# Kernel tuning notes

Measured on AMD Instinct MI355X. Metric: run time of the kernel, lower is better.

The kernel has to match this reference:

```python
import jax, jax.numpy as jnp
import numpy as np

N, K, F, NRBF = 10000, 32, 128, 300
GAMMA = 10.0


def ssp(x):
    # shifted softplus: softplus(x) - log(2)
    return jax.nn.softplus(x) - jnp.log(2.0).astype(x.dtype)


def setup_inputs() -> dict:
    key = jax.random.key(0)
    ks = jax.random.split(key, 12)
    s = lambda fan_in: 1.0 / np.sqrt(fan_in)
    inp = {
        "xyz": jax.random.normal(ks[0], (N, 3), jnp.float32) * 5.0,
        "atomic": jax.random.normal(ks[1], (N, F), jnp.float32),
        "edge_mask": (jax.random.uniform(ks[2], (N, K)) < 0.9).astype(jnp.float32),
        "src": jax.random.randint(ks[3], (N, K), 0, N),
        # pre_conv Linear(F, F) with bias
        "W_pre": jax.random.uniform(ks[4], (F, F), jnp.float32, -s(F), s(F)),
        "b_pre": jax.random.uniform(ks[5], (F,), jnp.float32, -s(F), s(F)),
        # cfconv: Linear(300, F, bias=False), SSP, Linear(F, F, bias=False), SSP
        "W_cf1": jax.random.uniform(ks[6], (NRBF, F), jnp.float32, -s(NRBF), s(NRBF)),
        "W_cf2": jax.random.uniform(ks[7], (F, F), jnp.float32, -s(F), s(F)),
        # post_conv: Linear(F,F), SSP, Linear(F,F)
        "W_post1": jax.random.uniform(ks[8], (F, F), jnp.float32, -s(F), s(F)),
        "b_post1": jax.random.uniform(ks[9], (F,), jnp.float32, -s(F), s(F)),
        "W_post2": jax.random.uniform(ks[10], (F, F), jnp.float32, -s(F), s(F)),
        "b_post2": jax.random.uniform(ks[11], (F,), jnp.float32, -s(F), s(F)),
        "rbf_centers": jnp.linspace(0.1, 30.1, NRBF, dtype=jnp.float32),
    }
    return inp


def reference(xyz, atomic, edge_mask, src, W_pre, b_pre, W_cf1, W_cf2,
              W_post1, b_post1, W_post2, b_post2, rbf_centers):
    pre = atomic @ W_pre + b_pre                       # [N, F]
    nbr_xyz = xyz[src]                                 # gather: [N, K, 3]
    d_ij = jnp.linalg.norm(nbr_xyz - xyz[:, None, :], axis=2, keepdims=True)  # [N, K, 1]
    rbf = jnp.exp(-GAMMA * (d_ij - rbf_centers[None, None, :]) ** 2)          # [N, K, 300]
    filters = ssp(ssp(rbf @ W_cf1) @ W_cf2)            # [N, K, F]
    conv_out = jnp.sum(filters * pre[src] * edge_mask[:, :, None], axis=1)    # [N, F]
    post = ssp(conv_out @ W_post1 + b_post1) @ W_post2 + b_post2
    return atomic + post
```

## Files before the change

### kernel.cpp

```cpp
#include <hip/hip_runtime.h>

#define NATOMS 10000
#define KNB 32
#define FD 128
#define NRBF 300
#define STEPC (30.0f / 299.0f)
#define INVSTEP (299.0f / 30.0f)
#define TROWS 256

typedef short short8 __attribute__((ext_vector_type(8)));
typedef float f32x4 __attribute__((ext_vector_type(4)));
typedef unsigned int u32x4 __attribute__((ext_vector_type(4)));

__device__ __forceinline__ unsigned short f2bf_rne(float f) {
    unsigned int u = __float_as_uint(f);
    u = (u + 0x7fffu + ((u >> 16) & 1u)) >> 16;
    return (unsigned short)u;
}

__device__ __forceinline__ unsigned int pack_bf2(float hi, float lo) {
    return __builtin_amdgcn_perm(__float_as_uint(hi) + 0x8000u,
                                 __float_as_uint(lo) + 0x8000u, 0x07060302u);
}

__device__ __forceinline__ unsigned short f2bf_rhu(float f) {
    return (unsigned short)((__float_as_uint(f) + 0x8000u) >> 16);
}

__device__ __forceinline__ float ssp_fast(float x) {
    float t = __builtin_amdgcn_exp2f(x * 1.44269504f);
    float l = __builtin_amdgcn_logf(1.0f + t);
    return 0.69314718056f * (l - 1.0f);
}

__device__ __forceinline__ float ssp_poly(float x) {
    float u = x * x;
    float p = fmaf(u, 2.1356923e-6f, -2.6351976e-5f);
    p = fmaf(u, p, 3.2552083e-4f);
    p = fmaf(u, p, -5.2083333e-3f);
    p = fmaf(u, p, 0.125f);
    return fmaf(0.5f, x, u * p);
}

__device__ __forceinline__ void gload_lds16(const void* g, void* l) {
    __builtin_amdgcn_global_load_lds(
        (const __attribute__((address_space(1))) unsigned int*)g,
        (__attribute__((address_space(3))) unsigned int*)l, 16, 0, 0);
}

__device__ __forceinline__ short8 rbf_row8(float d, float cg) {
    float t = d - cg;
    t = fminf(3.5f, fmaxf(-3.5f, t));
    float r = __builtin_amdgcn_exp2f(-14.4269504f * t * t);
    float q = __builtin_amdgcn_exp2f((28.8539008f * STEPC) * t
                                     - (14.4269504f * STEPC * STEPC));
    const float QRATIO = 0.81763172f;
    u32x4 p;
#pragma unroll
    for (int jj = 0; jj < 4; ++jj) {
        float v0 = r; r *= q; q *= QRATIO;
        float v1 = r; r *= q; q *= QRATIO;
        p[jj] = pack_bf2(v1, v0);
    }
    return __builtin_bit_cast(short8, p);
}

__global__ __launch_bounds__(256) void prep_pack(
    const float* __restrict__ Wcf1, const float* __restrict__ Wpre,
    const float* __restrict__ Wcf2, const float* __restrict__ Wpost1,
    const float* __restrict__ Wpost2, unsigned short* __restrict__ w1p,
    unsigned short* __restrict__ w4p) {
    int idx = blockIdx.x * 256 + threadIdx.x;
    if (idx < 40960) {
        int j = idx & 7, c = (idx >> 3) & 127, g = (idx >> 10) & 3, kc = idx >> 12;
        int k = kc * 32 + g * 8 + j;
        float v = (k < NRBF) ? Wcf1[k * FD + c] : 0.f;
        w1p[idx] = f2bf_rne(v);
    } else if (idx < 40960 + 65536) {
        int t = idx - 40960;
        int sel = t >> 14;
        int t2 = t & 16383;
        int j = t2 & 7, c = (t2 >> 3) & 127, g = (t2 >> 10) & 3, kc = t2 >> 12;
        int k = kc * 32 + g * 8 + j;
        const float* W = (sel == 0) ? Wpre : (sel == 1) ? Wcf2 : (sel == 2) ? Wpost1 : Wpost2;
        w4p[t] = f2bf_rne(W[k * FD + c]);
    }
}

__global__ __launch_bounds__(256) void pre_and_table(
    const float* __restrict__ X, const unsigned short* __restrict__ Wp,
    const float* __restrict__ bias, unsigned int* __restrict__ preP,
    const unsigned short* __restrict__ w1p, const unsigned short* __restrict__ w2p,
    unsigned int* __restrict__ T) {
    __shared__ unsigned short A2[128][132];
    const int tid = threadIdx.x;
    const int w = tid >> 6, lane = tid & 63, g = lane >> 4, c16 = lane & 15;

    if (blockIdx.x < 157) {
        const int r0 = blockIdx.x * 64 + w * 16;
        f32x4 acc[8];
#pragma unroll
        for (int b = 0; b < 8; ++b) acc[b] = (f32x4){0.f, 0.f, 0.f, 0.f};
        int row = r0 + c16;
        if (row >= NATOMS) row = 0;
#pragma unroll
        for (int kc = 0; kc < 4; ++kc) {
            const float* p0 = X + (size_t)row * FD + kc * 32 + g * 8;
            float4 xa = *(const float4*)p0, xb = *(const float4*)(p0 + 4);
            u32x4 pa;
            pa[0] = pack_bf2(xa.y, xa.x); pa[1] = pack_bf2(xa.w, xa.z);
            pa[2] = pack_bf2(xb.y, xb.x); pa[3] = pack_bf2(xb.w, xb.z);
            short8 a0 = __builtin_bit_cast(short8, pa);
            const unsigned short* wb = Wp + (kc * 4 + g) * 1024 + c16 * 8;
#pragma unroll
            for (int nb = 0; nb < 8; ++nb) {
                short8 b = *(const short8*)(wb + nb * 128);
                acc[nb] = __builtin_amdgcn_mfma_f32_16x16x32_bf16(a0, b, acc[nb], 0, 0, 0);
            }
        }
        float bv[8];
#pragma unroll
        for (int nb = 0; nb < 8; ++nb) bv[nb] = bias[nb * 16 + c16];
#pragma unroll
        for (int q = 0; q < 4; ++q) {
            int orow = r0 + 4 * g + q;
            if (orow < NATOMS) {
#pragma unroll
                for (int p2 = 0; p2 < 4; ++p2) {
                    float v0 = acc[2 * p2][q] + bv[2 * p2];
                    float v1 = acc[2 * p2 + 1][q] + bv[2 * p2 + 1];
                    preP[orow * 64 + c16 * 4 + p2] = pack_bf2(v1, v0);
                }
            }
        }
        return;
    }

    const int rbase = (int)(blockIdx.x - 157) * 128 + w * 32;
    const float hstep = 0.125f;
    const float d0 = (float)(rbase + c16) * hstep;
    const float d1 = (float)(rbase + 16 + c16) * hstep;

    const float BAND = 1.05f;
    float lo = (float)rbase * hstep, hi = (float)(rbase + 31) * hstep;
    int L = max(0, (int)floorf(((lo - BAND - 0.1f) * INVSTEP - 31.f) * 0.03125f));
    int H = min(9, (int)floorf(((hi + BAND - 0.1f) * INVSTEP) * 0.03125f));

    f32x4 acc[2][8];
#pragma unroll
    for (int a = 0; a < 2; ++a)
#pragma unroll
        for (int b = 0; b < 8; ++b) acc[a][b] = (f32x4){0.f, 0.f, 0.f, 0.f};

    for (int kc = L; kc <= H; ++kc) {
        const unsigned short* wb = w1p + kc * 4096 + g * 1024 + c16 * 8;
        short8 bfr[8];
#pragma unroll
        for (int nb = 0; nb < 8; ++nb) bfr[nb] = *(const short8*)(wb + nb * 128);
        const float cg = 0.1f + (float)(kc * 32 + g * 8) * STEPC;
        short8 a0 = rbf_row8(d0, cg);
        short8 a1 = rbf_row8(d1, cg);
#pragma unroll
        for (int nb = 0; nb < 8; ++nb) {
            acc[0][nb] = __builtin_amdgcn_mfma_f32_16x16x32_bf16(a0, bfr[nb], acc[0][nb], 0, 0, 0);
            acc[1][nb] = __builtin_amdgcn_mfma_f32_16x16x32_bf16(a1, bfr[nb], acc[1][nb], 0, 0, 0);
        }
    }

#pragma unroll
    for (int mr = 0; mr < 2; ++mr)
#pragma unroll
        for (int nb = 0; nb < 8; ++nb)
#pragma unroll
            for (int q = 0; q < 4; ++q) {
                int row = w * 32 + mr * 16 + 4 * g + q;
                A2[row][nb * 16 + c16] = f2bf_rhu(ssp_poly(acc[mr][nb][q]));
            }

    f32x4 acc2[2][8];
#pragma unroll
    for (int a = 0; a < 2; ++a)
#pragma unroll
        for (int b = 0; b < 8; ++b) acc2[a][b] = (f32x4){0.f, 0.f, 0.f, 0.f};

#pragma unroll
    for (int kc = 0; kc < 4; ++kc) {
        short8 a0 = *(const short8*)&A2[w * 32 + c16][kc * 32 + g * 8];
        short8 a1 = *(const short8*)&A2[w * 32 + 16 + c16][kc * 32 + g * 8];
        const unsigned short* wb = w2p + (kc * 4 + g) * 1024 + c16 * 8;
#pragma unroll
        for (int nb = 0; nb < 8; ++nb) {
            short8 b = *(const short8*)(wb + nb * 128);
            acc2[0][nb] = __builtin_amdgcn_mfma_f32_16x16x32_bf16(a0, b, acc2[0][nb], 0, 0, 0);
            acc2[1][nb] = __builtin_amdgcn_mfma_f32_16x16x32_bf16(a1, b, acc2[1][nb], 0, 0, 0);
        }
    }

#pragma unroll
    for (int mr = 0; mr < 2; ++mr)
#pragma unroll
        for (int q = 0; q < 4; ++q) {
            int r = rbase + mr * 16 + 4 * g + q;
#pragma unroll
            for (int p2 = 0; p2 < 4; ++p2) {
                float F0 = ssp_poly(acc2[mr][2 * p2][q]);
                float F1 = ssp_poly(acc2[mr][2 * p2 + 1][q]);
                T[r * 64 + c16 * 4 + p2] =
                    ((unsigned int)f2bf_rne(F1) << 16) | f2bf_rne(F0);
            }
        }
}

__global__ __launch_bounds__(512, 2) void conv_post(
    const float* __restrict__ xyz, const int* __restrict__ src,
    const float* __restrict__ mask, const unsigned int* __restrict__ preP,
    const unsigned int* __restrict__ T, const unsigned short* __restrict__ w1,
    const float* __restrict__ b1, const unsigned short* __restrict__ w2,
    const float* __restrict__ b2, const float* __restrict__ resid,
    float* __restrict__ Y) {
    __shared__ unsigned int Tl[TROWS * 64];
    __shared__ unsigned short Aconv[16][132];

    const int tid = threadIdx.x;
    const int w = tid >> 6;
    const int lane = tid & 63;
    const int l5 = lane & 31;
    const int c16 = lane & 15;
    const int g = lane >> 4;

#pragma unroll
    for (int it = 0; it < 8; ++it) {
        const unsigned int* gp = T + w * 2048 + it * 256 + lane * 4;
        gload_lds16(gp, &Tl[w * 2048 + it * 256]);
    }

    const int iA = blockIdx.x * 16 + w;
    const int iB = iA + 8;

    int svA = src[iA * KNB + l5];
    int svB = src[iB * KNB + l5];
    float mvA = mask[iA * KNB + l5];
    float mvB = mask[iB * KNB + l5];
    float dxA = xyz[3 * svA]     - xyz[3 * iA];
    float dyA = xyz[3 * svA + 1] - xyz[3 * iA + 1];
    float dzA = xyz[3 * svA + 2] - xyz[3 * iA + 2];
    float dxB = xyz[3 * svB]     - xyz[3 * iB];
    float dyB = xyz[3 * svB + 1] - xyz[3 * iB + 1];
    float dzB = xyz[3 * svB + 2] - xyz[3 * iB + 2];
    float dA = sqrtf(dxA * dxA + dyA * dyA + dzA * dzA);
    float dB = sqrtf(dxB * dxB + dyB * dyB + dzB * dzB);
    dA = (mvA > 0.f) ? dA : 1e9f;
    dB = (mvB > 0.f) ? dB : 1e9f;
    float tA = fminf(dA * 8.0f, (float)(TROWS - 2) + 0.999f);
    float tB = fminf(dB * 8.0f, (float)(TROWS - 2) + 0.999f);
    float fiA = floorf(tA), fiB = floorf(tB);
    float frA = tA - fiA,  frB = tB - fiB;
    int iiA = (int)fiA, iiB = (int)fiB;

    __syncthreads();

    float a00 = 0.f, a01 = 0.f, a10 = 0.f, a11 = 0.f;
#pragma unroll
    for (int e = 0; e < KNB; ++e) {
        int   ie0 = __builtin_amdgcn_readlane(iiA, e);
        int   se0 = __builtin_amdgcn_readlane(svA, e);
        float fe0 = __uint_as_float((unsigned int)__builtin_amdgcn_readlane(
                        (int)__float_as_uint(frA), e));
        int   ie1 = __builtin_amdgcn_readlane(iiB, e);
        int   se1 = __builtin_amdgcn_readlane(svB, e);
        float fe1 = __uint_as_float((unsigned int)__builtin_amdgcn_readlane(
                        (int)__float_as_uint(frB), e));
        unsigned int tvA0 = Tl[ie0 * 64 + lane];
        unsigned int tvB0 = Tl[ie0 * 64 + 64 + lane];
        unsigned int tvA1 = Tl[ie1 * 64 + lane];
        unsigned int tvB1 = Tl[ie1 * 64 + 64 + lane];
        unsigned int pw0 = preP[se0 * 64 + lane];
        unsigned int pw1 = preP[se1 * 64 + lane];
        float A00 = __uint_as_float(tvA0 << 16);
        float A01 = __uint_as_float(tvA0 & 0xffff0000u);
        float B00 = __uint_as_float(tvB0 << 16);
        float B01 = __uint_as_float(tvB0 & 0xffff0000u);
        float f00 = fmaf(fe0, B00 - A00, A00);
        float f01 = fmaf(fe0, B01 - A01, A01);
        a00 = fmaf(f00, __uint_as_float(pw0 << 16), a00);
        a01 = fmaf(f01, __uint_as_float(pw0 & 0xffff0000u), a01);
        float A10 = __uint_as_float(tvA1 << 16);
        float A11 = __uint_as_float(tvA1 & 0xffff0000u);
        float B10 = __uint_as_float(tvB1 << 16);
        float B11 = __uint_as_float(tvB1 & 0xffff0000u);
        float f10 = fmaf(fe1, B10 - A10, A10);
        float f11 = fmaf(fe1, B11 - A11, A11);
        a10 = fmaf(f10, __uint_as_float(pw1 << 16), a10);
        a11 = fmaf(f11, __uint_as_float(pw1 & 0xffff0000u), a11);
    }
    {
        int c0 = 32 * (lane & 3) + (lane >> 2);
        Aconv[w][c0]          = f2bf_rhu(a00);
        Aconv[w][c0 + 16]     = f2bf_rhu(a01);
        Aconv[w + 8][c0]      = f2bf_rhu(a10);
        Aconv[w + 8][c0 + 16] = f2bf_rhu(a11);
    }
    __syncthreads();

    unsigned short* Amid = (unsigned short*)Tl;
    const int r0 = blockIdx.x * 16;

    f32x4 acc = (f32x4){0.f, 0.f, 0.f, 0.f};
#pragma unroll
    for (int kc = 0; kc < 4; ++kc) {
        short8 a0 = *(const short8*)&Aconv[c16][kc * 32 + g * 8];
        const unsigned short* wb = w1 + (kc * 4 + g) * 1024;
        short8 b = *(const short8*)(wb + (w * 16 + c16) * 8);
        acc = __builtin_amdgcn_mfma_f32_16x16x32_bf16(a0, b, acc, 0, 0, 0);
    }
    {
        float bv = b1[w * 16 + c16];
#pragma unroll
        for (int q = 0; q < 4; ++q)
            Amid[(4 * g + q) * 132 + w * 16 + c16] =
                f2bf_rhu(ssp_fast(acc[q] + bv));
    }
    __syncthreads();

    f32x4 acc2 = (f32x4){0.f, 0.f, 0.f, 0.f};
#pragma unroll
    for (int kc = 0; kc < 4; ++kc) {
        short8 a0 = *(const short8*)&Amid[c16 * 132 + kc * 32 + g * 8];
        const unsigned short* wb = w2 + (kc * 4 + g) * 1024;
        short8 b = *(const short8*)(wb + (w * 16 + c16) * 8);
        acc2 = __builtin_amdgcn_mfma_f32_16x16x32_bf16(a0, b, acc2, 0, 0, 0);
    }
    {
        float bv2 = b2[w * 16 + c16];
#pragma unroll
        for (int q = 0; q < 4; ++q) {
            int o = (r0 + 4 * g + q) * FD + w * 16 + c16;
            Y[o] = acc2[q] + bv2 + resid[o];
        }
    }
}

extern "C" void kernel_launch(void* const* d_in, const int* in_sizes, int n_in,
                              void* d_out, int out_size, void* d_ws, size_t ws_size,
                              hipStream_t stream) {
    const float* xyz     = (const float*)d_in[0];
    const float* atomic  = (const float*)d_in[1];
    const float* mask    = (const float*)d_in[2];
    const int*   src     = (const int*)d_in[3];
    const float* W_pre   = (const float*)d_in[4];
    const float* b_pre   = (const float*)d_in[5];
    const float* W_cf1   = (const float*)d_in[6];
    const float* W_cf2   = (const float*)d_in[7];
    const float* W_post1 = (const float*)d_in[8];
    const float* b_post1 = (const float*)d_in[9];
    const float* W_post2 = (const float*)d_in[10];
    const float* b_post2 = (const float*)d_in[11];
    float* out = (float*)d_out;

    unsigned int*   preP = (unsigned int*)d_ws;
    unsigned short* w1p  = (unsigned short*)((char*)d_ws + 7680000);
    unsigned short* w4p  = w1p + 40960;
    unsigned int*   T    = (unsigned int*)((char*)d_ws + 7892992);
    unsigned short* wpre   = w4p;
    unsigned short* wcf2   = w4p + 16384;
    unsigned short* wpost1 = w4p + 32768;
    unsigned short* wpost2 = w4p + 49152;

    prep_pack<<<416, 256, 0, stream>>>(W_cf1, W_pre, W_cf2, W_post1, W_post2, w1p, w4p);
    pre_and_table<<<159, 256, 0, stream>>>(atomic, wpre, b_pre, preP, w1p, wcf2, T);
    conv_post<<<625, 512, 0, stream>>>(xyz, src, mask, preP, T,
                                       wpost1, b_post1, wpost2, b_post2, atomic, out);
}
```

Before: 40.27 us.

## Fold weight packing into pre/table kernel and batch neighbor gathers

Removes the separate weight-packing kernel. The pre-linear and RBF-table blocks now read fp32 weights directly and convert them to bf16 fragments on the fly. Dedicated extra blocks pack the post weights, and the pre GEMM is split across twice as many blocks with half the output columns per wave. The conv loop is restructured to issue eight neighbors' table and preP loads before consuming them, which raises memory-level parallelism at the cost of more registers. The changes cut one kernel launch but add strided, uncoalesced fp32 weight reads inside the compute kernels.

```diff
diff --git a/kernel.cpp b/kernel.cpp
--- a/kernel.cpp
+++ b/kernel.cpp
@@ -65,44 +65,50 @@
     return __builtin_bit_cast(short8, p);
 }
 
-__global__ __launch_bounds__(256) void prep_pack(
-    const float* __restrict__ Wcf1, const float* __restrict__ Wpre,
-    const float* __restrict__ Wcf2, const float* __restrict__ Wpost1,
-    const float* __restrict__ Wpost2, unsigned short* __restrict__ w1p,
-    unsigned short* __restrict__ w4p) {
-    int idx = blockIdx.x * 256 + threadIdx.x;
-    if (idx < 40960) {
-        int j = idx & 7, c = (idx >> 3) & 127, g = (idx >> 10) & 3, kc = idx >> 12;
-        int k = kc * 32 + g * 8 + j;
-        float v = (k < NRBF) ? Wcf1[k * FD + c] : 0.f;
-        w1p[idx] = f2bf_rne(v);
-    } else if (idx < 40960 + 65536) {
-        int t = idx - 40960;
-        int sel = t >> 14;
-        int t2 = t & 16383;
-        int j = t2 & 7, c = (t2 >> 3) & 127, g = (t2 >> 10) & 3, kc = t2 >> 12;
-        int k = kc * 32 + g * 8 + j;
-        const float* W = (sel == 0) ? Wpre : (sel == 1) ? Wcf2 : (sel == 2) ? Wpost1 : Wpost2;
-        w4p[t] = f2bf_rne(W[k * FD + c]);
-    }
-}
-
-__global__ __launch_bounds__(256) void pre_and_table(
-    const float* __restrict__ X, const unsigned short* __restrict__ Wp,
+__device__ __forceinline__ short8 load_bfrag_f32(const float* __restrict__ W,
+                                                 int k0, int c) {
+    u32x4 p;
+#pragma unroll
+    for (int jj = 0; jj < 4; ++jj) {
+        int ka = k0 + 2 * jj;
+        p[jj] = pack_bf2(W[(ka + 1) * FD + c], W[ka * FD + c]);
+    }
+    return __builtin_bit_cast(short8, p);
+}
+
+__device__ __forceinline__ short8 load_bfrag_f32_g(const float* __restrict__ W,
+                                                   int k0, int c, int kmax) {
+    u32x4 p;
+#pragma unroll
+    for (int jj = 0; jj < 4; ++jj) {
+        int ka = k0 + 2 * jj;
+        float va = (ka < kmax) ? W[ka * FD + c] : 0.f;
+        float vb = (ka + 1 < kmax) ? W[(ka + 1) * FD + c] : 0.f;
+        p[jj] = pack_bf2(vb, va);
+    }
+    return __builtin_bit_cast(short8, p);
+}
+
+__global__ __launch_bounds__(256) void pre_table_pack(
+    const float* __restrict__ X, const float* __restrict__ Wpre,
     const float* __restrict__ bias, unsigned int* __restrict__ preP,
-    const unsigned short* __restrict__ w1p, const unsigned short* __restrict__ w2p,
-    unsigned int* __restrict__ T) {
+    const float* __restrict__ Wcf1, const float* __restrict__ Wcf2,
+    unsigned int* __restrict__ T, const float* __restrict__ Wpost1,
+    const float* __restrict__ Wpost2, unsigned short* __restrict__ wp) {
     __shared__ unsigned short A2[128][132];
     const int tid = threadIdx.x;
     const int w = tid >> 6, lane = tid & 63, g = lane >> 4, c16 = lane & 15;
 
-    if (blockIdx.x < 157) {
-        const int r0 = blockIdx.x * 64 + w * 16;
-        f32x4 acc[8];
-#pragma unroll
-        for (int b = 0; b < 8; ++b) acc[b] = (f32x4){0.f, 0.f, 0.f, 0.f};
-        int row = r0 + c16;
+    if (blockIdx.x < 313) {
+        const int r0b = blockIdx.x * 32;
+        const int r = w >> 1, c = w & 1;
+        int row = r0b + r * 16 + c16;
         if (row >= NATOMS) row = 0;
+
+        f32x4 acc[4];
+#pragma unroll
+        for (int b = 0; b < 4; ++b) acc[b] = (f32x4){0.f, 0.f, 0.f, 0.f};
+
 #pragma unroll
         for (int kc = 0; kc < 4; ++kc) {
             const float* p0 = X + (size_t)row * FD + kc * 32 + g * 8;
@@ -111,32 +117,45 @@
             pa[0] = pack_bf2(xa.y, xa.x); pa[1] = pack_bf2(xa.w, xa.z);
             pa[2] = pack_bf2(xb.y, xb.x); pa[3] = pack_bf2(xb.w, xb.z);
             short8 a0 = __builtin_bit_cast(short8, pa);
-            const unsigned short* wb = Wp + (kc * 4 + g) * 1024 + c16 * 8;
-#pragma unroll
-            for (int nb = 0; nb < 8; ++nb) {
-                short8 b = *(const short8*)(wb + nb * 128);
+            int k0 = kc * 32 + g * 8;
+#pragma unroll
+            for (int nb = 0; nb < 4; ++nb) {
+                short8 b = load_bfrag_f32(Wpre, k0, (c * 4 + nb) * 16 + c16);
                 acc[nb] = __builtin_amdgcn_mfma_f32_16x16x32_bf16(a0, b, acc[nb], 0, 0, 0);
             }
         }
-        float bv[8];
-#pragma unroll
-        for (int nb = 0; nb < 8; ++nb) bv[nb] = bias[nb * 16 + c16];
+
+        float bv[4];
+#pragma unroll
+        for (int nb = 0; nb < 4; ++nb) bv[nb] = bias[(c * 4 + nb) * 16 + c16];
 #pragma unroll
         for (int q = 0; q < 4; ++q) {
-            int orow = r0 + 4 * g + q;
+            int orow = r0b + r * 16 + 4 * g + q;
             if (orow < NATOMS) {
 #pragma unroll
-                for (int p2 = 0; p2 < 4; ++p2) {
-                    float v0 = acc[2 * p2][q] + bv[2 * p2];
-                    float v1 = acc[2 * p2 + 1][q] + bv[2 * p2 + 1];
-                    preP[orow * 64 + c16 * 4 + p2] = pack_bf2(v1, v0);
+                for (int pp = 0; pp < 2; ++pp) {
+                    float v0 = acc[2 * pp][q] + bv[2 * pp];
+                    float v1 = acc[2 * pp + 1][q] + bv[2 * pp + 1];
+                    preP[orow * 64 + c16 * 4 + c * 2 + pp] = pack_bf2(v1, v0);
                 }
             }
         }
         return;
     }
 
-    const int rbase = (int)(blockIdx.x - 157) * 128 + w * 32;
+    if (blockIdx.x >= 315) {
+        const int sel = blockIdx.x - 315;
+        const float* W = sel ? Wpost2 : Wpost1;
+        unsigned short* o = wp + sel * 16384;
+        for (int t2 = tid; t2 < 16384; t2 += 256) {
+            int j = t2 & 7, cc = (t2 >> 3) & 127, gg = (t2 >> 10) & 3, kc = t2 >> 12;
+            int k = kc * 32 + gg * 8 + j;
+            o[t2] = f2bf_rne(W[k * FD + cc]);
+        }
+        return;
+    }
+
+    const int rbase = (int)(blockIdx.x - 313) * 128 + w * 32;
     const float hstep = 0.125f;
     const float d0 = (float)(rbase + c16) * hstep;
     const float d1 = (float)(rbase + 16 + c16) * hstep;
@@ -153,11 +172,12 @@
         for (int b = 0; b < 8; ++b) acc[a][b] = (f32x4){0.f, 0.f, 0.f, 0.f};
 
     for (int kc = L; kc <= H; ++kc) {
-        const unsigned short* wb = w1p + kc * 4096 + g * 1024 + c16 * 8;
+        int k0 = kc * 32 + g * 8;
         short8 bfr[8];
 #pragma unroll
-        for (int nb = 0; nb < 8; ++nb) bfr[nb] = *(const short8*)(wb + nb * 128);
-        const float cg = 0.1f + (float)(kc * 32 + g * 8) * STEPC;
+        for (int nb = 0; nb < 8; ++nb)
+            bfr[nb] = load_bfrag_f32_g(Wcf1, k0, nb * 16 + c16, NRBF);
+        const float cg = 0.1f + (float)k0 * STEPC;
         short8 a0 = rbf_row8(d0, cg);
         short8 a1 = rbf_row8(d1, cg);
 #pragma unroll
@@ -187,10 +207,9 @@
     for (int kc = 0; kc < 4; ++kc) {
         short8 a0 = *(const short8*)&A2[w * 32 + c16][kc * 32 + g * 8];
         short8 a1 = *(const short8*)&A2[w * 32 + 16 + c16][kc * 32 + g * 8];
-        const unsigned short* wb = w2p + (kc * 4 + g) * 1024 + c16 * 8;
 #pragma unroll
         for (int nb = 0; nb < 8; ++nb) {
-            short8 b = *(const short8*)(wb + nb * 128);
+            short8 b = load_bfrag_f32(Wcf2, kc * 32 + g * 8, nb * 16 + c16);
             acc2[0][nb] = __builtin_amdgcn_mfma_f32_16x16x32_bf16(a0, b, acc2[0][nb], 0, 0, 0);
             acc2[1][nb] = __builtin_amdgcn_mfma_f32_16x16x32_bf16(a1, b, acc2[1][nb], 0, 0, 0);
         }
@@ -200,12 +219,12 @@
     for (int mr = 0; mr < 2; ++mr)
 #pragma unroll
         for (int q = 0; q < 4; ++q) {
-            int r = rbase + mr * 16 + 4 * g + q;
+            int rr = rbase + mr * 16 + 4 * g + q;
 #pragma unroll
             for (int p2 = 0; p2 < 4; ++p2) {
                 float F0 = ssp_poly(acc2[mr][2 * p2][q]);
                 float F1 = ssp_poly(acc2[mr][2 * p2 + 1][q]);
-                T[r * 64 + c16 * 4 + p2] =
+                T[rr * 64 + c16 * 4 + p2] =
                     ((unsigned int)f2bf_rne(F1) << 16) | f2bf_rne(F0);
             }
         }
@@ -261,37 +280,46 @@
 
     float a00 = 0.f, a01 = 0.f, a10 = 0.f, a11 = 0.f;
 #pragma unroll
-    for (int e = 0; e < KNB; ++e) {
-        int   ie0 = __builtin_amdgcn_readlane(iiA, e);
-        int   se0 = __builtin_amdgcn_readlane(svA, e);
-        float fe0 = __uint_as_float((unsigned int)__builtin_amdgcn_readlane(
-                        (int)__float_as_uint(frA), e));
-        int   ie1 = __builtin_amdgcn_readlane(iiB, e);
-        int   se1 = __builtin_amdgcn_readlane(svB, e);
-        float fe1 = __uint_as_float((unsigned int)__builtin_amdgcn_readlane(
-                        (int)__float_as_uint(frB), e));
-        unsigned int tvA0 = Tl[ie0 * 64 + lane];
-        unsigned int tvB0 = Tl[ie0 * 64 + 64 + lane];
-        unsigned int tvA1 = Tl[ie1 * 64 + lane];
-        unsigned int tvB1 = Tl[ie1 * 64 + 64 + lane];
-        unsigned int pw0 = preP[se0 * 64 + lane];
-        unsigned int pw1 = preP[se1 * 64 + lane];
-        float A00 = __uint_as_float(tvA0 << 16);
-        float A01 = __uint_as_float(tvA0 & 0xffff0000u);
-        float B00 = __uint_as_float(tvB0 << 16);
-        float B01 = __uint_as_float(tvB0 & 0xffff0000u);
-        float f00 = fmaf(fe0, B00 - A00, A00);
-        float f01 = fmaf(fe0, B01 - A01, A01);
-        a00 = fmaf(f00, __uint_as_float(pw0 << 16), a00);
-        a01 = fmaf(f01, __uint_as_float(pw0 & 0xffff0000u), a01);
-        float A10 = __uint_as_float(tvA1 << 16);
-        float A11 = __uint_as_float(tvA1 & 0xffff0000u);
-        float B10 = __uint_as_float(tvB1 << 16);
-        float B11 = __uint_as_float(tvB1 & 0xffff0000u);
-        float f10 = fmaf(fe1, B10 - A10, A10);
-        float f11 = fmaf(fe1, B11 - A11, A11);
-        a10 = fmaf(f10, __uint_as_float(pw1 << 16), a10);
-        a11 = fmaf(f11, __uint_as_float(pw1 & 0xffff0000u), a11);
+    for (int eb = 0; eb < KNB; eb += 8) {
+        unsigned int tA0[8], tB0[8], tA1[8], tB1[8], q0[8], q1[8];
+        float fr0[8], fr1[8];
+#pragma unroll
+        for (int j = 0; j < 8; ++j) {
+            const int e = eb + j;
+            int ie0 = __builtin_amdgcn_readlane(iiA, e);
+            int se0 = __builtin_amdgcn_readlane(svA, e);
+            fr0[j] = __uint_as_float((unsigned int)__builtin_amdgcn_readlane(
+                         (int)__float_as_uint(frA), e));
+            int ie1 = __builtin_amdgcn_readlane(iiB, e);
+            int se1 = __builtin_amdgcn_readlane(svB, e);
+            fr1[j] = __uint_as_float((unsigned int)__builtin_amdgcn_readlane(
+                         (int)__float_as_uint(frB), e));
+            q0[j] = preP[se0 * 64 + lane];
+            q1[j] = preP[se1 * 64 + lane];
+            tA0[j] = Tl[ie0 * 64 + lane];
+            tB0[j] = Tl[ie0 * 64 + 64 + lane];
+            tA1[j] = Tl[ie1 * 64 + lane];
+            tB1[j] = Tl[ie1 * 64 + 64 + lane];
+        }
+#pragma unroll
+        for (int j = 0; j < 8; ++j) {
+            float A00 = __uint_as_float(tA0[j] << 16);
+            float A01 = __uint_as_float(tA0[j] & 0xffff0000u);
+            float B00 = __uint_as_float(tB0[j] << 16);
+            float B01 = __uint_as_float(tB0[j] & 0xffff0000u);
+            float f00 = fmaf(fr0[j], B00 - A00, A00);
+            float f01 = fmaf(fr0[j], B01 - A01, A01);
+            a00 = fmaf(f00, __uint_as_float(q0[j] << 16), a00);
+            a01 = fmaf(f01, __uint_as_float(q0[j] & 0xffff0000u), a01);
+            float A10 = __uint_as_float(tA1[j] << 16);
+            float A11 = __uint_as_float(tA1[j] & 0xffff0000u);
+            float B10 = __uint_as_float(tB1[j] << 16);
+            float B11 = __uint_as_float(tB1[j] & 0xffff0000u);
+            float f10 = fmaf(fr1[j], B10 - A10, A10);
+            float f11 = fmaf(fr1[j], B11 - A11, A11);
+            a10 = fmaf(f10, __uint_as_float(q1[j] << 16), a10);
+            a11 = fmaf(f11, __uint_as_float(q1[j] & 0xffff0000u), a11);
+        }
     }
     {
         int c0 = 32 * (lane & 3) + (lane >> 2);
@@ -358,16 +386,11 @@
     float* out = (float*)d_out;
 
     unsigned int*   preP = (unsigned int*)d_ws;
-    unsigned short* w1p  = (unsigned short*)((char*)d_ws + 7680000);
-    unsigned short* w4p  = w1p + 40960;
-    unsigned int*   T    = (unsigned int*)((char*)d_ws + 7892992);
-    unsigned short* wpre   = w4p;
-    unsigned short* wcf2   = w4p + 16384;
-    unsigned short* wpost1 = w4p + 32768;
-    unsigned short* wpost2 = w4p + 49152;
-
-    prep_pack<<<416, 256, 0, stream>>>(W_cf1, W_pre, W_cf2, W_post1, W_post2, w1p, w4p);
-    pre_and_table<<<159, 256, 0, stream>>>(atomic, wpre, b_pre, preP, w1p, wcf2, T);
+    unsigned int*   T    = (unsigned int*)((char*)d_ws + 2560000);
+    unsigned short* wp   = (unsigned short*)((char*)d_ws + 2625536);
+
+    pre_table_pack<<<317, 256, 0, stream>>>(atomic, W_pre, b_pre, preP,
+                                            W_cf1, W_cf2, T, W_post1, W_post2, wp);
     conv_post<<<625, 512, 0, stream>>>(xyz, src, mask, preP, T,
-                                       wpost1, b_post1, wpost2, b_post2, atomic, out);
-}
+                                       wp, b_post1, wp + 16384, b_post2, atomic, out);
+}
```

Measured after the change: 80.94 us. +101.0%, slower.

## Process 20 atoms per conv_post block with 10 waves and a smaller table

Applied to the files above, without the earlier changes.

Shrinks the distance lookup table to 252 rows and changes conv_post to 640-thread blocks that each handle 20 atoms, giving 500 blocks instead of 625. The per-block table load into LDS is spread across 10 waves. The post MLP now runs on 8 waves using two 16-row MFMA tiles over zero-padded rows. This amortises the LDS table fill over more atoms per block and changes occupancy, at the cost of wasted MFMA work on padding rows and two idle waves during the MLP. The workspace layout is also moved.

```diff
diff --git a/kernel.cpp b/kernel.cpp
--- a/kernel.cpp
+++ b/kernel.cpp
@@ -6,7 +6,7 @@
 #define NRBF 300
 #define STEPC (30.0f / 299.0f)
 #define INVSTEP (299.0f / 30.0f)
-#define TROWS 256
+#define TROWS 252
 
 typedef short short8 __attribute__((ext_vector_type(8)));
 typedef float f32x4 __attribute__((ext_vector_type(4)));
@@ -201,17 +201,19 @@
 #pragma unroll
         for (int q = 0; q < 4; ++q) {
             int r = rbase + mr * 16 + 4 * g + q;
-#pragma unroll
-            for (int p2 = 0; p2 < 4; ++p2) {
-                float F0 = ssp_poly(acc2[mr][2 * p2][q]);
-                float F1 = ssp_poly(acc2[mr][2 * p2 + 1][q]);
-                T[r * 64 + c16 * 4 + p2] =
-                    ((unsigned int)f2bf_rne(F1) << 16) | f2bf_rne(F0);
-            }
-        }
-}
-
-__global__ __launch_bounds__(512, 2) void conv_post(
+            if (r < TROWS) {
+#pragma unroll
+                for (int p2 = 0; p2 < 4; ++p2) {
+                    float F0 = ssp_poly(acc2[mr][2 * p2][q]);
+                    float F1 = ssp_poly(acc2[mr][2 * p2 + 1][q]);
+                    T[r * 64 + c16 * 4 + p2] =
+                        ((unsigned int)f2bf_rne(F1) << 16) | f2bf_rne(F0);
+                }
+            }
+        }
+}
+
+__global__ __launch_bounds__(640, 5) void conv_post(
     const float* __restrict__ xyz, const int* __restrict__ src,
     const float* __restrict__ mask, const unsigned int* __restrict__ preP,
     const unsigned int* __restrict__ T, const unsigned short* __restrict__ w1,
@@ -219,7 +221,7 @@
     const float* __restrict__ b2, const float* __restrict__ resid,
     float* __restrict__ Y) {
     __shared__ unsigned int Tl[TROWS * 64];
-    __shared__ unsigned short Aconv[16][132];
+    __shared__ unsigned short Aconv[32][132];
 
     const int tid = threadIdx.x;
     const int w = tid >> 6;
@@ -229,13 +231,17 @@
     const int g = lane >> 4;
 
 #pragma unroll
-    for (int it = 0; it < 8; ++it) {
-        const unsigned int* gp = T + w * 2048 + it * 256 + lane * 4;
-        gload_lds16(gp, &Tl[w * 2048 + it * 256]);
-    }
-
-    const int iA = blockIdx.x * 16 + w;
-    const int iB = iA + 8;
+    for (int it = 0; it < 7; ++it) {
+        int chunk = w * 7 + it;
+        if (chunk < 63) {
+            const unsigned int* gp = T + chunk * 256 + lane * 4;
+            gload_lds16(gp, &Tl[chunk * 256]);
+        }
+    }
+
+    const int base = blockIdx.x * 20;
+    const int iA = base + w;
+    const int iB = iA + 10;
 
     int svA = src[iA * KNB + l5];
     int svB = src[iB * KNB + l5];
@@ -295,48 +301,65 @@
     }
     {
         int c0 = 32 * (lane & 3) + (lane >> 2);
-        Aconv[w][c0]          = f2bf_rhu(a00);
-        Aconv[w][c0 + 16]     = f2bf_rhu(a01);
-        Aconv[w + 8][c0]      = f2bf_rhu(a10);
-        Aconv[w + 8][c0 + 16] = f2bf_rhu(a11);
-    }
+        Aconv[w][c0]           = f2bf_rhu(a00);
+        Aconv[w][c0 + 16]      = f2bf_rhu(a01);
+        Aconv[w + 10][c0]      = f2bf_rhu(a10);
+        Aconv[w + 10][c0 + 16] = f2bf_rhu(a11);
+    }
+
+    for (int idx = tid; idx < 12 * 132; idx += 640)
+        (&Aconv[20][0])[idx] = 0;
+
     __syncthreads();
 
     unsigned short* Amid = (unsigned short*)Tl;
-    const int r0 = blockIdx.x * 16;
-
-    f32x4 acc = (f32x4){0.f, 0.f, 0.f, 0.f};
-#pragma unroll
-    for (int kc = 0; kc < 4; ++kc) {
-        short8 a0 = *(const short8*)&Aconv[c16][kc * 32 + g * 8];
-        const unsigned short* wb = w1 + (kc * 4 + g) * 1024;
-        short8 b = *(const short8*)(wb + (w * 16 + c16) * 8);
-        acc = __builtin_amdgcn_mfma_f32_16x16x32_bf16(a0, b, acc, 0, 0, 0);
-    }
-    {
+    if (w < 8) {
+        f32x4 acc[2];
+        acc[0] = (f32x4){0.f, 0.f, 0.f, 0.f};
+        acc[1] = (f32x4){0.f, 0.f, 0.f, 0.f};
+#pragma unroll
+        for (int kc = 0; kc < 4; ++kc) {
+            short8 a0 = *(const short8*)&Aconv[c16][kc * 32 + g * 8];
+            short8 a1 = *(const short8*)&Aconv[16 + c16][kc * 32 + g * 8];
+            const unsigned short* wb = w1 + (kc * 4 + g) * 1024;
+            short8 b = *(const short8*)(wb + (w * 16 + c16) * 8);
+            acc[0] = __builtin_amdgcn_mfma_f32_16x16x32_bf16(a0, b, acc[0], 0, 0, 0);
+            acc[1] = __builtin_amdgcn_mfma_f32_16x16x32_bf16(a1, b, acc[1], 0, 0, 0);
+        }
         float bv = b1[w * 16 + c16];
 #pragma unroll
-        for (int q = 0; q < 4; ++q)
-            Amid[(4 * g + q) * 132 + w * 16 + c16] =
-                f2bf_rhu(ssp_fast(acc[q] + bv));
+        for (int mr = 0; mr < 2; ++mr)
+#pragma unroll
+            for (int q = 0; q < 4; ++q)
+                Amid[(mr * 16 + 4 * g + q) * 132 + w * 16 + c16] =
+                    f2bf_rhu(ssp_fast(acc[mr][q] + bv));
     }
     __syncthreads();
 
-    f32x4 acc2 = (f32x4){0.f, 0.f, 0.f, 0.f};
-#pragma unroll
-    for (int kc = 0; kc < 4; ++kc) {
-        short8 a0 = *(const short8*)&Amid[c16 * 132 + kc * 32 + g * 8];
-        const unsigned short* wb = w2 + (kc * 4 + g) * 1024;
-        short8 b = *(const short8*)(wb + (w * 16 + c16) * 8);
-        acc2 = __builtin_amdgcn_mfma_f32_16x16x32_bf16(a0, b, acc2, 0, 0, 0);
-    }
-    {
+    if (w < 8) {
+        f32x4 acc2[2];
+        acc2[0] = (f32x4){0.f, 0.f, 0.f, 0.f};
+        acc2[1] = (f32x4){0.f, 0.f, 0.f, 0.f};
+#pragma unroll
+        for (int kc = 0; kc < 4; ++kc) {
+            short8 a0 = *(const short8*)&Amid[c16 * 132 + kc * 32 + g * 8];
+            short8 a1 = *(const short8*)&Amid[(16 + c16) * 132 + kc * 32 + g * 8];
+            const unsigned short* wb = w2 + (kc * 4 + g) * 1024;
+            short8 b = *(const short8*)(wb + (w * 16 + c16) * 8);
+            acc2[0] = __builtin_amdgcn_mfma_f32_16x16x32_bf16(a0, b, acc2[0], 0, 0, 0);
+            acc2[1] = __builtin_amdgcn_mfma_f32_16x16x32_bf16(a1, b, acc2[1], 0, 0, 0);
+        }
         float bv2 = b2[w * 16 + c16];
 #pragma unroll
-        for (int q = 0; q < 4; ++q) {
-            int o = (r0 + 4 * g + q) * FD + w * 16 + c16;
-            Y[o] = acc2[q] + bv2 + resid[o];
-        }
+        for (int mr = 0; mr < 2; ++mr)
+#pragma unroll
+            for (int q = 0; q < 4; ++q) {
+                int rl = mr * 16 + 4 * g + q;
+                if (rl < 20) {
+                    int o = (base + rl) * FD + w * 16 + c16;
+                    Y[o] = acc2[mr][q] + bv2 + resid[o];
+                }
+            }
     }
 }
 
@@ -358,9 +381,9 @@
     float* out = (float*)d_out;
 
     unsigned int*   preP = (unsigned int*)d_ws;
-    unsigned short* w1p  = (unsigned short*)((char*)d_ws + 7680000);
+    unsigned int*   T    = (unsigned int*)((char*)d_ws + 2560000);
+    unsigned short* w1p  = (unsigned short*)((char*)d_ws + 2625536);
     unsigned short* w4p  = w1p + 40960;
-    unsigned int*   T    = (unsigned int*)((char*)d_ws + 7892992);
     unsigned short* wpre   = w4p;
     unsigned short* wcf2   = w4p + 16384;
     unsigned short* wpost1 = w4p + 32768;
@@ -368,6 +391,6 @@
 
     prep_pack<<<416, 256, 0, stream>>>(W_cf1, W_pre, W_cf2, W_post1, W_post2, w1p, w4p);
     pre_and_table<<<159, 256, 0, stream>>>(atomic, wpre, b_pre, preP, w1p, wcf2, T);
-    conv_post<<<625, 512, 0, stream>>>(xyz, src, mask, preP, T,
+    conv_post<<<500, 640, 0, stream>>>(xyz, src, mask, preP, T,
                                        wpost1, b_post1, wpost2, b_post2, atomic, out);
 }
```

Result: slower. 44.32 us (+10.0%).
